# Kernel optimization log

Hardware: AMD Instinct MI355X
Metric: run time of the kernel (lower is better)

The kernel has to match this reference:

```python
import jax, jax.numpy as jnp
import numpy as np

B, T, C, H = 8, 1024, 768, 12
D = C // H  # head_dim = 64

def _rope_tables(seq_len, d, base=10000.0):
    inv_freq = 1.0 / (base ** (jnp.arange(0, d, 2, dtype=jnp.float32) / d))  # [d/2]
    freqs = jnp.outer(jnp.arange(seq_len, dtype=jnp.float32), inv_freq)      # [T, d/2]
    return jnp.cos(freqs), jnp.sin(freqs)

def _apply_rotary(x, cos, sin):
    # x: [B,T,H,D]; cos/sin: [1,T,1,D/2]
    d = x.shape[-1] // 2
    x1, x2 = x[..., :d], x[..., d:]
    return jnp.concatenate([x1 * cos + x2 * sin, -x1 * sin + x2 * cos], axis=-1)

def setup_inputs() -> dict:
    key = jax.random.key(0)
    k1, k2, k3 = jax.random.split(key, 3)
    x = jax.random.normal(k1, (B, T, C), dtype=jnp.float32)
    w_qkv = jax.random.normal(k2, (3 * C, C), dtype=jnp.float32) * (C ** -0.5)
    w_proj = jax.random.normal(k3, (C, C), dtype=jnp.float32) * (C ** -0.5)
    return {"x": x, "w_qkv": w_qkv, "w_proj": w_proj}

def reference(x, w_qkv, w_proj):
    Bb, Tt, Cc = x.shape
    qkv = x @ w_qkv.T                                   # [B,T,3C]
    q, k, v = jnp.split(qkv, 3, axis=2)
    q = q.reshape(Bb, Tt, H, D)
    k = k.reshape(Bb, Tt, H, D)
    v = v.reshape(Bb, Tt, H, D)
    cos, sin = _rope_tables(Tt, D)
    cos = cos[None, :, None, :]
    sin = sin[None, :, None, :]
    q = _apply_rotary(q, cos, sin)
    k = _apply_rotary(k, cos, sin)
    scale = 1.0 / jnp.sqrt(jnp.float32(D))
    scores = jnp.einsum('bthd,bshd->bhts', q, k) * scale  # [B,H,T,T]
    causal = jnp.tril(jnp.ones((Tt, Tt), dtype=bool))
    scores = jnp.where(causal[None, None], scores, jnp.finfo(scores.dtype).min)
    p = jax.nn.softmax(scores, axis=-1)
    y = jnp.einsum('bhts,bshd->bthd', p, v).reshape(Bb, Tt, Cc)
    return y @ w_proj.T
```

## Files before the change

kernel.cpp:

```cpp
#include <hip/hip_runtime.h>
#include <hip/hip_bf16.h>

#define Bb 8
#define Tt 1024
#define Cc 768
#define Hh 12
#define Dd 64
#define M_ROWS (Bb * Tt)
#define QKV_N (3 * Cc)

typedef __attribute__((ext_vector_type(8))) short s16x8;
typedef __attribute__((ext_vector_type(4))) short s16x4;
typedef __attribute__((ext_vector_type(4))) float f32x4;

#define AS1 __attribute__((address_space(1)))
#define AS3 __attribute__((address_space(3)))

static __device__ __forceinline__ short f2bf(float f) {
    union { float f; unsigned u; } v; v.f = f;
    unsigned r = (v.u + 0x7fffu + ((v.u >> 16) & 1u)) >> 16;
    return (short)r;
}

static __device__ __forceinline__ void cast8(const float* __restrict__ in,
                                             short* __restrict__ out, int i) {
    const float4 a = ((const float4*)in)[i * 2];
    const float4 b = ((const float4*)in)[i * 2 + 1];
    s16x8 f;
    f[0] = f2bf(a.x); f[1] = f2bf(a.y); f[2] = f2bf(a.z); f[3] = f2bf(a.w);
    f[4] = f2bf(b.x); f[5] = f2bf(b.y); f[6] = f2bf(b.z); f[7] = f2bf(b.w);
    ((s16x8*)out)[i] = f;
}

#define S1 (M_ROWS * Cc / 8)
#define S2 (QKV_N * Cc / 8)
#define S3 (Cc * Cc / 8)
#define SROPE (Tt * 32)
#define PREP_THREADS (S1 + S2 + S3 + SROPE)

__global__ __launch_bounds__(256) void prep_kernel(const float* __restrict__ x,
                                                   const float* __restrict__ wqkv,
                                                   const float* __restrict__ wproj,
                                                   short* __restrict__ xb,
                                                   short* __restrict__ wqkvb,
                                                   short* __restrict__ wprojb,
                                                   float2* __restrict__ cs) {
    int idx = blockIdx.x * blockDim.x + threadIdx.x;
    if (idx < S1) { cast8(x, xb, idx); return; }
    idx -= S1;
    if (idx < S2) { cast8(wqkv, wqkvb, idx); return; }
    idx -= S2;
    if (idx < S3) { cast8(wproj, wprojb, idx); return; }
    idx -= S3;
    {
        int t = idx >> 5, i = idx & 31;
        float inv_freq = exp2f(-0.41524101186092037f * (float)i);
        float fr = (float)t * inv_freq;
        float2 v; v.x = cosf(fr); v.y = sinf(fr);
        cs[idx] = v;
    }
}

template <int MODE, int TN>
__global__ __launch_bounds__(256, 3) void gemm_nt_mfma(const short* __restrict__ A,
                                                       const short* __restrict__ B,
                                                       void* __restrict__ Cout,
                                                       const float2* __restrict__ cs,
                                                       int M, int N, int K, int nblocks) {
    __shared__ short As[2][128 * 32];
    __shared__ short Bs[2][TN * 32];
    constexpr int NT = TN / 16;

    const int wave = threadIdx.x >> 6;
    const int lane = threadIdx.x & 63;
    const int l16  = lane & 15;
    const int quad = lane >> 4;

    const int mb8  = (M >> 7) >> 3;
    const int xcd  = blockIdx.x & 7;
    const int slot = blockIdx.x >> 3;
    const int bm = (xcd * mb8 + slot / nblocks) * 128;
    const int bn = (slot % nblocks) * TN;

    f32x4 acc[2][NT] = {};

    auto stage = [&](int k0, int buf) {
#pragma unroll
        for (int j = 0; j < 2; j++) {
            const int D = j * 256 + wave * 64 + lane;
            const int G = D >> 3;
            const int s = (G << 3) | ((D & 7) ^ (G & 7));
            const int m = s >> 2, c4 = (s & 3) * 8;
            __builtin_amdgcn_global_load_lds(
                (const AS1 unsigned*)(A + (size_t)(bm + m) * K + k0 + c4),
                (AS3 unsigned*)&As[buf][(j * 256 + wave * 64) * 8], 16, 0, 0);
        }
#pragma unroll
        for (int j = 0; j < TN / 64; j++) {
            const int D = j * 256 + wave * 64 + lane;
            const int G = D >> 3;
            const int s = (G << 3) | ((D & 7) ^ (G & 7));
            const int m = s >> 2, c4 = (s & 3) * 8;
            __builtin_amdgcn_global_load_lds(
                (const AS1 unsigned*)(B + (size_t)(bn + m) * K + k0 + c4),
                (AS3 unsigned*)&Bs[buf][(j * 256 + wave * 64) * 8], 16, 0, 0);
        }
    };

    const int nIter = K >> 5;
    stage(0, 0);
    for (int kt = 0; kt < nIter; kt++) {
        const int buf = kt & 1;
        __syncthreads();
        if (kt + 1 < nIter) stage((kt + 1) << 5, buf ^ 1);

        s16x8 af[2];
#pragma unroll
        for (int mt = 0; mt < 2; mt++) {
            const int m = wave * 32 + mt * 16 + l16;
            const int d = ((m & 1) * 4 + quad) ^ ((m >> 1) & 7);
            af[mt] = *(const s16x8*)&As[buf][(m >> 1) * 64 + d * 8];
        }
#pragma unroll
        for (int nt = 0; nt < NT; nt++) {
            const int n = nt * 16 + l16;
            const int d = ((n & 1) * 4 + quad) ^ ((n >> 1) & 7);
            s16x8 bf = *(const s16x8*)&Bs[buf][(n >> 1) * 64 + d * 8];
            acc[0][nt] = __builtin_amdgcn_mfma_f32_16x16x32_bf16(af[0], bf, acc[0][nt], 0, 0, 0);
            acc[1][nt] = __builtin_amdgcn_mfma_f32_16x16x32_bf16(af[1], bf, acc[1][nt], 0, 0, 0);
        }
    }

    if constexpr (MODE == 0) {
#pragma unroll
        for (int mt = 0; mt < 2; mt++)
#pragma unroll
            for (int r = 0; r < 4; r++) {
                const size_t row = bm + wave * 32 + mt * 16 + quad * 4 + r;
#pragma unroll
                for (int nt = 0; nt < NT; nt++)
                    ((float*)Cout)[row * N + bn + nt * 16 + l16] = acc[mt][nt][r];
            }
    } else {
        const bool is_v = (bn >= 2 * Cc);
        if (is_v) {
#pragma unroll
            for (int mt = 0; mt < 2; mt++)
#pragma unroll
                for (int r = 0; r < 4; r++) {
                    const size_t row = bm + wave * 32 + mt * 16 + quad * 4 + r;
#pragma unroll
                    for (int nt = 0; nt < NT; nt++)
                        ((short*)Cout)[row * N + bn + nt * 16 + l16] = f2bf(acc[mt][nt][r]);
                }
        } else {
            const float scale = (bn < Cc) ? 0.125f : 1.0f;
#pragma unroll
            for (int mt = 0; mt < 2; mt++) {
#pragma unroll
                for (int r = 0; r < 4; r++) {
                    const int row = bm + wave * 32 + mt * 16 + quad * 4 + r;
                    const int t = row & (Tt - 1);
                    const float2 c0 = cs[t * 32 + l16];
                    const float2 c1 = cs[t * 32 + 16 + l16];
#pragma unroll
                    for (int hh = 0; hh < TN / 64; hh++) {
                        const float x0 = acc[mt][hh * 4 + 0][r];
                        const float x1 = acc[mt][hh * 4 + 1][r];
                        const float x2 = acc[mt][hh * 4 + 2][r];
                        const float x3 = acc[mt][hh * 4 + 3][r];
                        short* cp = (short*)Cout + (size_t)row * N + bn + hh * 64;
                        cp[l16]      = f2bf((x0 * c0.x + x2 * c0.y) * scale);
                        cp[16 + l16] = f2bf((x1 * c1.x + x3 * c1.y) * scale);
                        cp[32 + l16] = f2bf((-x0 * c0.y + x2 * c0.x) * scale);
                        cp[48 + l16] = f2bf((-x1 * c1.y + x3 * c1.x) * scale);
                    }
                }
            }
        }
    }
}

#define KSP 72
#define VSP 72
#define PP  76

__global__ __launch_bounds__(256) void flash_attn(const short* __restrict__ qkv,
                                                  short* __restrict__ y) {
    __shared__ short Ks[2][64 * KSP];
    __shared__ short Vs[2][Dd * VSP];
    __shared__ short Ps[4][16 * PP];

    const int wave = threadIdx.x >> 6;
    const int lane = threadIdx.x & 63;
    const int l16  = lane & 15;
    const int quad = lane >> 4;

    const int pair = blockIdx.x / 96;
    const int bh   = blockIdx.x % 96;
    const int h = bh % Hh;
    const int b = bh / Hh;
    const int qa_blk = pair;
    const int qb_blk = 15 - pair;
    const int q0a = qa_blk * 64 + wave * 16;
    const int q0b = qb_blk * 64 + wave * 16;

    s16x8 qfa[2], qfb[2];
    {
        const short* qpa = qkv + (size_t)(b * Tt + q0a + l16) * QKV_N + h * Dd + quad * 8;
        const short* qpb = qkv + (size_t)(b * Tt + q0b + l16) * QKV_N + h * Dd + quad * 8;
        qfa[0] = *(const s16x8*)qpa;  qfa[1] = *(const s16x8*)(qpa + 32);
        qfb[0] = *(const s16x8*)qpb;  qfb[1] = *(const s16x8*)(qpb + 32);
    }

    f32x4 oa[4] = {}, ob[4] = {};
    float la[4] = {0.f, 0.f, 0.f, 0.f}, lb[4] = {0.f, 0.f, 0.f, 0.f};

    short* pw = &Ps[wave][0];

    const int krow = threadIdx.x >> 2;
    const int kd0  = (threadIdx.x & 3) * 16;
    const int key2 = (threadIdx.x & 31) * 2;
    const int dv0  = (threadIdx.x >> 5) * 8;

    s16x8 pk0, pk1, pv0, pv1;
    auto load_tile = [&](int kbase) {
        const short* kp = qkv + (size_t)(b * Tt + kbase + krow) * QKV_N + Cc + h * Dd + kd0;
        pk0 = *(const s16x8*)kp;
        pk1 = *(const s16x8*)(kp + 8);
        const short* vp = qkv + (size_t)(b * Tt + kbase + key2) * QKV_N + 2 * Cc + h * Dd + dv0;
        pv0 = *(const s16x8*)vp;
        pv1 = *(const s16x8*)(vp + QKV_N);
    };
    auto store_tile = [&](int buf) {
        *(s16x8*)&Ks[buf][krow * KSP + kd0]     = pk0;
        *(s16x8*)&Ks[buf][krow * KSP + kd0 + 8] = pk1;
#pragma unroll
        for (int j = 0; j < 8; j++) {
            ushort2 w; w.x = (unsigned short)pv0[j]; w.y = (unsigned short)pv1[j];
            *(ushort2*)&Vs[buf][(dv0 + j) * VSP + key2] = w;
        }
    };

    auto process = [&](int buf, int q0, const s16x8* qf, f32x4* o, float* l_r,
                       int kbase, bool masked) {
        f32x4 sv[4];
#pragma unroll
        for (int g = 0; g < 4; g++) {
            s16x8 kf0 = *(const s16x8*)&Ks[buf][(g * 16 + l16) * KSP + quad * 8];
            s16x8 kf1 = *(const s16x8*)&Ks[buf][(g * 16 + l16) * KSP + 32 + quad * 8];
            f32x4 z = {};
            z = __builtin_amdgcn_mfma_f32_16x16x32_bf16(qf[0], kf0, z, 0, 0, 0);
            z = __builtin_amdgcn_mfma_f32_16x16x32_bf16(qf[1], kf1, z, 0, 0, 0);
            sv[g] = z;
        }
#pragma unroll
        for (int r = 0; r < 4; r++) {
            const int qg = q0 + quad * 4 + r;
            float rs = 0.f;
#pragma unroll
            for (int g = 0; g < 4; g++) {
                float p = __expf(sv[g][r]);
                if (masked) p = (kbase + g * 16 + l16 <= qg) ? p : 0.0f;
                rs += p;
                pw[(quad * 4 + r) * PP + g * 16 + l16] = f2bf(p);
            }
            l_r[r] += rs;
        }
#pragma unroll
        for (int c = 0; c < 2; c++) {
            s16x4 plo = *(const s16x4*)&pw[l16 * PP + c * 32 + quad * 8];
            s16x4 phi = *(const s16x4*)&pw[l16 * PP + c * 32 + quad * 8 + 4];
            s16x8 pa = __builtin_shufflevector(plo, phi, 0, 1, 2, 3, 4, 5, 6, 7);
#pragma unroll
            for (int nc = 0; nc < 4; nc++) {
                s16x8 vb = *(const s16x8*)&Vs[buf][(nc * 16 + l16) * VSP + c * 32 + quad * 8];
                o[nc] = __builtin_amdgcn_mfma_f32_16x16x32_bf16(pa, vb, o[nc], 0, 0, 0);
            }
        }
    };

    load_tile(0);
    store_tile(0);
    for (int kt = 0; kt <= qb_blk; kt++) {
        __syncthreads();
        const int nb = (kt < qb_blk) ? (kt + 1) * 64 : qb_blk * 64;
        load_tile(nb);
        const int buf = kt & 1;
        const int kbase = kt * 64;
        process(buf, q0b, qfb, ob, lb, kbase, kt == qb_blk);
        if (kt <= qa_blk)
            process(buf, q0a, qfa, oa, la, kbase, kt == qa_blk);
        store_tile(buf ^ 1);
    }

#pragma unroll
    for (int r = 0; r < 4; r++) {
        float sa = la[r], sb = lb[r];
#pragma unroll
        for (int off = 1; off < 16; off <<= 1) {
            sa += __shfl_xor(sa, off, 64);
            sb += __shfl_xor(sb, off, 64);
        }
        const float inva = 1.0f / sa;
        const float invb = 1.0f / sb;
        short* ypa = y + (size_t)(b * Tt + q0a + quad * 4 + r) * Cc + h * Dd;
        short* ypb = y + (size_t)(b * Tt + q0b + quad * 4 + r) * Cc + h * Dd;
#pragma unroll
        for (int nc = 0; nc < 4; nc++) {
            ypa[nc * 16 + l16] = f2bf(oa[nc][r] * inva);
            ypb[nc * 16 + l16] = f2bf(ob[nc][r] * invb);
        }
    }
}

extern "C" void kernel_launch(void* const* d_in, const int* in_sizes, int n_in,
                              void* d_out, int out_size, void* d_ws, size_t ws_size,
                              hipStream_t stream) {
    const float* x      = (const float*)d_in[0];
    const float* w_qkv  = (const float*)d_in[1];
    const float* w_proj = (const float*)d_in[2];
    float* out = (float*)d_out;

    float2* cs    = (float2*)d_ws;
    short* xb     = (short*)(cs + Tt * 32);
    short* wqkvb  = xb + (size_t)M_ROWS * Cc;
    short* wprojb = wqkvb + (size_t)QKV_N * Cc;
    short* qkvb   = wprojb + (size_t)Cc * Cc;
    short* yb     = qkvb + (size_t)M_ROWS * QKV_N;

    prep_kernel<<<PREP_THREADS / 256, 256, 0, stream>>>(
        x, w_qkv, w_proj, xb, wqkvb, wprojb, cs);

    gemm_nt_mfma<1, 192><<<768, 256, 0, stream>>>(
        xb, wqkvb, qkvb, cs, M_ROWS, QKV_N, Cc, QKV_N / 192);

    flash_attn<<<96 * 8, 256, 0, stream>>>(qkvb, yb);

    gemm_nt_mfma<0, 128><<<384, 256, 0, stream>>>(
        yb, wprojb, out, nullptr, M_ROWS, Cc, Cc, Cc / 128);
}
```

Baseline: 175.2 us.

## Transpose attention MFMA operands, reuse K buffer for P, retile projection GEMM

The attention kernel now computes S^T = K·Q^T and O^T = V·P^T. Each lane then holds four consecutive keys for a single query. P can be written with packed 4-element stores and read back as one 8-element vector, and the output is stored with vectorized writes. The row-sum reduction drops from four values and four shuffle rounds to one value and two shuffles. The separate P scratch array is removed in favour of the idle K double-buffer half, which each wave owns by row. The output projection GEMM also moves from a 128-wide to a 96-wide N tile with 512 blocks, with a guarded B-staging loop for non-multiple chunk counts.

```diff
diff --git a/kernel.cpp b/kernel.cpp
--- a/kernel.cpp
+++ b/kernel.cpp
@@ -95,15 +95,18 @@
                 (const AS1 unsigned*)(A + (size_t)(bm + m) * K + k0 + c4),
                 (AS3 unsigned*)&As[buf][(j * 256 + wave * 64) * 8], 16, 0, 0);
         }
-#pragma unroll
-        for (int j = 0; j < TN / 64; j++) {
-            const int D = j * 256 + wave * 64 + lane;
-            const int G = D >> 3;
-            const int s = (G << 3) | ((D & 7) ^ (G & 7));
-            const int m = s >> 2, c4 = (s & 3) * 8;
-            __builtin_amdgcn_global_load_lds(
-                (const AS1 unsigned*)(B + (size_t)(bn + m) * K + k0 + c4),
-                (AS3 unsigned*)&Bs[buf][(j * 256 + wave * 64) * 8], 16, 0, 0);
+        constexpr int BCH = TN * 4;
+#pragma unroll
+        for (int j = 0; j < (BCH + 255) / 256; j++) {
+            if (BCH % 256 == 0 || j * 256 + wave * 64 < BCH) {
+                const int D = j * 256 + wave * 64 + lane;
+                const int G = D >> 3;
+                const int s = (G << 3) | ((D & 7) ^ (G & 7));
+                const int m = s >> 2, c4 = (s & 3) * 8;
+                __builtin_amdgcn_global_load_lds(
+                    (const AS1 unsigned*)(B + (size_t)(bn + m) * K + k0 + c4),
+                    (AS3 unsigned*)&Bs[buf][(j * 256 + wave * 64) * 8], 16, 0, 0);
+            }
         }
     };
 
@@ -183,13 +186,11 @@
 
 #define KSP 72
 #define VSP 72
-#define PP  76
 
 __global__ __launch_bounds__(256) void flash_attn(const short* __restrict__ qkv,
                                                   short* __restrict__ y) {
     __shared__ short Ks[2][64 * KSP];
     __shared__ short Vs[2][Dd * VSP];
-    __shared__ short Ps[4][16 * PP];
 
     const int wave = threadIdx.x >> 6;
     const int lane = threadIdx.x & 63;
@@ -214,9 +215,7 @@
     }
 
     f32x4 oa[4] = {}, ob[4] = {};
-    float la[4] = {0.f, 0.f, 0.f, 0.f}, lb[4] = {0.f, 0.f, 0.f, 0.f};
-
-    short* pw = &Ps[wave][0];
+    float la = 0.f, lb = 0.f;
 
     const int krow = threadIdx.x >> 2;
     const int kd0  = (threadIdx.x & 3) * 16;
@@ -242,40 +241,42 @@
         }
     };
 
-    auto process = [&](int buf, int q0, const s16x8* qf, f32x4* o, float* l_r,
+    auto process = [&](int buf, int q0, const s16x8* qf, f32x4* o, float& l_acc,
                        int kbase, bool masked) {
-        f32x4 sv[4];
+        short* pw = &Ks[buf ^ 1][wave * 16 * KSP];
+        f32x4 e[4];
 #pragma unroll
         for (int g = 0; g < 4; g++) {
             s16x8 kf0 = *(const s16x8*)&Ks[buf][(g * 16 + l16) * KSP + quad * 8];
             s16x8 kf1 = *(const s16x8*)&Ks[buf][(g * 16 + l16) * KSP + 32 + quad * 8];
             f32x4 z = {};
-            z = __builtin_amdgcn_mfma_f32_16x16x32_bf16(qf[0], kf0, z, 0, 0, 0);
-            z = __builtin_amdgcn_mfma_f32_16x16x32_bf16(qf[1], kf1, z, 0, 0, 0);
-            sv[g] = z;
-        }
-#pragma unroll
-        for (int r = 0; r < 4; r++) {
-            const int qg = q0 + quad * 4 + r;
-            float rs = 0.f;
-#pragma unroll
-            for (int g = 0; g < 4; g++) {
-                float p = __expf(sv[g][r]);
-                if (masked) p = (kbase + g * 16 + l16 <= qg) ? p : 0.0f;
+            z = __builtin_amdgcn_mfma_f32_16x16x32_bf16(kf0, qf[0], z, 0, 0, 0);
+            z = __builtin_amdgcn_mfma_f32_16x16x32_bf16(kf1, qf[1], z, 0, 0, 0);
+            e[g] = z;
+        }
+        float rs = 0.f;
+#pragma unroll
+        for (int g = 0; g < 4; g++) {
+#pragma unroll
+            for (int r = 0; r < 4; r++) {
+                float p = __expf(e[g][r]);
+                if (masked) p = (kbase + g * 16 + quad * 4 + r <= q0 + l16) ? p : 0.0f;
+                e[g][r] = p;
                 rs += p;
-                pw[(quad * 4 + r) * PP + g * 16 + l16] = f2bf(p);
-            }
-            l_r[r] += rs;
-        }
+            }
+            s16x4 pk;
+            pk[0] = f2bf(e[g][0]); pk[1] = f2bf(e[g][1]);
+            pk[2] = f2bf(e[g][2]); pk[3] = f2bf(e[g][3]);
+            *(s16x4*)&pw[l16 * KSP + g * 16 + quad * 4] = pk;
+        }
+        l_acc += rs;
 #pragma unroll
         for (int c = 0; c < 2; c++) {
-            s16x4 plo = *(const s16x4*)&pw[l16 * PP + c * 32 + quad * 8];
-            s16x4 phi = *(const s16x4*)&pw[l16 * PP + c * 32 + quad * 8 + 4];
-            s16x8 pa = __builtin_shufflevector(plo, phi, 0, 1, 2, 3, 4, 5, 6, 7);
+            s16x8 pb = *(const s16x8*)&pw[l16 * KSP + c * 32 + quad * 8];
 #pragma unroll
             for (int nc = 0; nc < 4; nc++) {
                 s16x8 vb = *(const s16x8*)&Vs[buf][(nc * 16 + l16) * VSP + c * 32 + quad * 8];
-                o[nc] = __builtin_amdgcn_mfma_f32_16x16x32_bf16(pa, vb, o[nc], 0, 0, 0);
+                o[nc] = __builtin_amdgcn_mfma_f32_16x16x32_bf16(vb, pb, o[nc], 0, 0, 0);
             }
         }
     };
@@ -294,23 +295,22 @@
         store_tile(buf ^ 1);
     }
 
-#pragma unroll
-    for (int r = 0; r < 4; r++) {
-        float sa = la[r], sb = lb[r];
-#pragma unroll
-        for (int off = 1; off < 16; off <<= 1) {
-            sa += __shfl_xor(sa, off, 64);
-            sb += __shfl_xor(sb, off, 64);
-        }
-        const float inva = 1.0f / sa;
-        const float invb = 1.0f / sb;
-        short* ypa = y + (size_t)(b * Tt + q0a + quad * 4 + r) * Cc + h * Dd;
-        short* ypb = y + (size_t)(b * Tt + q0b + quad * 4 + r) * Cc + h * Dd;
-#pragma unroll
-        for (int nc = 0; nc < 4; nc++) {
-            ypa[nc * 16 + l16] = f2bf(oa[nc][r] * inva);
-            ypb[nc * 16 + l16] = f2bf(ob[nc][r] * invb);
-        }
+    float sa = la; sa += __shfl_xor(sa, 16, 64); sa += __shfl_xor(sa, 32, 64);
+    float sb = lb; sb += __shfl_xor(sb, 16, 64); sb += __shfl_xor(sb, 32, 64);
+    const float inva = 1.0f / sa;
+    const float invb = 1.0f / sb;
+    short* ypa = y + (size_t)(b * Tt + q0a + l16) * Cc + h * Dd + quad * 4;
+    short* ypb = y + (size_t)(b * Tt + q0b + l16) * Cc + h * Dd + quad * 4;
+#pragma unroll
+    for (int nc = 0; nc < 4; nc++) {
+        s16x4 va, vb2;
+#pragma unroll
+        for (int r = 0; r < 4; r++) {
+            va[r]  = f2bf(oa[nc][r] * inva);
+            vb2[r] = f2bf(ob[nc][r] * invb);
+        }
+        *(s16x4*)&ypa[nc * 16] = va;
+        *(s16x4*)&ypb[nc * 16] = vb2;
     }
 }
 
@@ -337,6 +337,6 @@
 
     flash_attn<<<96 * 8, 256, 0, stream>>>(qkvb, yb);
 
-    gemm_nt_mfma<0, 128><<<384, 256, 0, stream>>>(
-        yb, wprojb, out, nullptr, M_ROWS, Cc, Cc, Cc / 128);
-}
+    gemm_nt_mfma<0, 96><<<512, 256, 0, stream>>>(
+        yb, wprojb, out, nullptr, M_ROWS, Cc, Cc, Cc / 96);
+}
```

After: 174.9 us. Within noise of the previous version (-0.2%).
